# Performance work log

Measured on AMD Instinct MI355X. Metric: run time of the kernel, lower is better.

The kernel has to match this reference:

```python
import jax, jax.numpy as jnp
import numpy as np

N_NODES = 100000
N_EDGES = 3200000
ALPHA_KCL = 1.0
ALPHA_KVL = 1.0
EPS = 1e-6


def setup_inputs() -> dict:
    key = jax.random.key(0)
    k1, k2, k3, k4 = jax.random.split(key, 4)
    node_features = jax.random.normal(k1, (N_NODES, 4), dtype=jnp.float32)
    edge_index = jax.random.randint(k2, (2, N_EDGES), 0, N_NODES, dtype=jnp.int64)
    edge_logits = jax.random.normal(k3, (N_EDGES,), dtype=jnp.float32)
    edge_params = jax.random.uniform(k4, (N_EDGES, 2), dtype=jnp.float32)
    return {
        "node_features": node_features,
        "edge_index": edge_index,
        "edge_logits": edge_logits,
        "edge_params": edge_params,
    }


def reference(node_features, edge_index, edge_logits, edge_params):
    n_nodes = node_features.shape[0]
    edge_probs = jax.nn.sigmoid(edge_logits)  # [E]
    src = edge_index[0]  # [E]
    dst = edge_index[1]  # [E]
    v = node_features[:, 0]  # [N] voltage column
    # per-edge current: |v_src - v_dst| / (R + X + eps) * prob
    v_diff = jnp.abs(v[src] - v[dst])
    impedance = edge_params[:, 0] + edge_params[:, 1]
    current = v_diff / (impedance + EPS) * edge_probs  # [E]
    # KCL: each edge subtracts its current at src, adds at dst
    node_sum = (
        jax.ops.segment_sum(current, dst, num_segments=n_nodes)
        - jax.ops.segment_sum(current, src, num_segments=n_nodes)
    )  # [N]
    kcl_loss = jnp.mean(node_sum ** 2)
    # KVL (simplified): mean of per-column unbiased variance of edge_params
    kvl_loss = jnp.var(edge_params, axis=0, ddof=1).mean()
    return ALPHA_KCL * kcl_loss + ALPHA_KVL * kvl_loss
```

## Files before the change

### kernel.cpp

```cpp
#include <hip/hip_runtime.h>
#include <math.h>

#define N_NODES 100000
#define N_EDGES 3200000
#define EPS_F 1e-6f

#define SLICE_N 12500
#define NSLICE  8
#define NCHUNK  32
#define C_PAIRS (N_EDGES / 2 / NCHUNK)
#define SBATCH  8

#define NVARB   6250
#define NKCLB   391

#define CNT_WORD  32
#define PK_OFF    64
#define PART_OFF  (PK_OFF + 2 * N_EDGES)
#define VARP_OFF  (PART_OFF + NCHUNK * N_NODES)
#define KCLP_OFF  (VARP_OFF + 4 * NVARB)
#define WS_FLOATS (KCLP_OFF + NKCLB + 64)

__device__ __forceinline__ float wave_reduce(float v) {
    #pragma unroll
    for (int off = 32; off > 0; off >>= 1) v += __shfl_down(v, off, 64);
    return v;
}

__device__ __forceinline__ void fadd_agent(float* p, float v) {
    unsafeAtomicAdd(p, v);
}

__device__ __forceinline__ unsigned short f2bf(float f) {
    unsigned u = __float_as_uint(f);
    unsigned r = ((u >> 16) & 1u) + 0x7FFFu;
    return (unsigned short)((u + r) >> 16);
}
__device__ __forceinline__ float bf2f(unsigned short h) {
    return __uint_as_float(((unsigned)h) << 16);
}

__global__ __launch_bounds__(256) void prep_kernel(
    const float*  __restrict__ nf,
    const void*   __restrict__ eidx,
    const float*  __restrict__ logits,
    const float2* __restrict__ params,
    float*        __restrict__ ws)
{
    __shared__ float red[4][4];
    const int* i32 = (const int*)eidx;

    int any = 0;
    #pragma unroll
    for (int k = 1; k < 32; k += 2) any |= i32[k];
    const bool is32 = (any != 0);

    const int t = blockIdx.x * blockDim.x + threadIdx.x;

    if (t == 0) ((unsigned*)ws)[CNT_WORD] = 0;

    int2 sp, dp;
    if (is32) {
        sp = ((const int2*)i32)[t];
        dp = ((const int2*)(i32 + N_EDGES))[t];
    } else {
        const int4 a = ((const int4*)i32)[t];
        const int4 b = ((const int4*)(i32 + 2 * N_EDGES))[t];
        sp = make_int2(a.x, a.z);
        dp = make_int2(b.x, b.z);
    }

    const float vs0 = nf[sp.x * 4];
    const float vd0 = nf[dp.x * 4];
    const float vs1 = nf[sp.y * 4];
    const float vd1 = nf[dp.y * 4];

    const float4 pp = ((const float4*)params)[t];
    const float2 lg = ((const float2*)logits)[t];
    const float w0 = (1.0f / (1.0f + __expf(-lg.x))) / (pp.x + pp.y + EPS_F);
    const float w1 = (1.0f / (1.0f + __expf(-lg.y))) / (pp.z + pp.w + EPS_F);
    const float c0 = fabsf(vs0 - vd0) * w0;
    const float c1 = fabsf(vs1 - vd1) * w1;

    int4 pk;
    pk.x = (int)((unsigned)sp.x | ((unsigned)dp.x << 17));
    pk.y = (int)((((unsigned)dp.x) >> 15) | ((unsigned)f2bf(c0) << 2));
    pk.z = (int)((unsigned)sp.y | ((unsigned)dp.y << 17));
    pk.w = (int)((((unsigned)dp.y) >> 15) | ((unsigned)f2bf(c1) << 2));
    ((int4*)(ws + PK_OFF))[t] = pk;

    float s0 = pp.x + pp.z;
    float s1 = pp.y + pp.w;
    float q0 = pp.x * pp.x + pp.z * pp.z;
    float q1 = pp.y * pp.y + pp.w * pp.w;

    s0 = wave_reduce(s0); s1 = wave_reduce(s1);
    q0 = wave_reduce(q0); q1 = wave_reduce(q1);

    const int wid = threadIdx.x >> 6;
    if ((threadIdx.x & 63) == 0) {
        red[wid][0] = s0; red[wid][1] = s1; red[wid][2] = q0; red[wid][3] = q1;
    }
    __syncthreads();
    if (threadIdx.x == 0) {
        float4 o;
        o.x = red[0][0] + red[1][0] + red[2][0] + red[3][0];
        o.y = red[0][1] + red[1][1] + red[2][1] + red[3][1];
        o.z = red[0][2] + red[1][2] + red[2][2] + red[3][2];
        o.w = red[0][3] + red[1][3] + red[2][3] + red[3][3];
        ((float4*)(ws + VARP_OFF))[blockIdx.x] = o;
    }
}

__global__ __launch_bounds__(1024) void scatter_kernel(float* __restrict__ ws)
{
    __shared__ float bins[SLICE_N];

    const int c  = blockIdx.x & (NCHUNK - 1);
    const int s  = blockIdx.x >> 5;
    const unsigned lo = (unsigned)(s * SLICE_N);

    for (int j = threadIdx.x; j < SLICE_N; j += 1024) bins[j] = 0.f;
    __syncthreads();

    const int4* pk = (const int4*)(ws + PK_OFF);

    const int p0 = c * C_PAIRS;
    const int p1 = p0 + C_PAIRS;

    for (int base = p0 + (int)threadIdx.x; base < p1; base += 1024 * SBATCH) {
        int4 q[SBATCH];
        #pragma unroll
        for (int k = 0; k < SBATCH; ++k) {
            int p = base + k * 1024;
            p = (p < p1) ? p : (p1 - 1);
            q[k] = pk[p];
        }
        #pragma unroll
        for (int k = 0; k < SBATCH; ++k) {
            const int p = base + k * 1024;
            if (p < p1) {
                const unsigned lo0 = (unsigned)q[k].x, hi0 = (unsigned)q[k].y;
                const unsigned lo1 = (unsigned)q[k].z, hi1 = (unsigned)q[k].w;
                const unsigned s0 = (lo0 & 0x1FFFFu) - lo;
                const unsigned d0 = ((lo0 >> 17) | ((hi0 & 3u) << 15)) - lo;
                const unsigned s1 = (lo1 & 0x1FFFFu) - lo;
                const unsigned d1 = ((lo1 >> 17) | ((hi1 & 3u) << 15)) - lo;
                const float c0 = bf2f((unsigned short)((hi0 >> 2) & 0xFFFFu));
                const float c1 = bf2f((unsigned short)((hi1 >> 2) & 0xFFFFu));
                if (d0 < SLICE_N) atomicAdd(&bins[d0],  c0);
                if (s0 < SLICE_N) atomicAdd(&bins[s0], -c0);
                if (d1 < SLICE_N) atomicAdd(&bins[d1],  c1);
                if (s1 < SLICE_N) atomicAdd(&bins[s1], -c1);
            }
        }
    }
    __syncthreads();

    float4* pt4 = (float4*)(ws + PART_OFF + (size_t)c * N_NODES + lo);
    for (int j = threadIdx.x; j < SLICE_N / 4; j += 1024)
        pt4[j] = ((const float4*)bins)[j];
}

__global__ __launch_bounds__(256) void kclfinal_kernel(float* __restrict__ ws,
                                                       float* __restrict__ out)
{
    __shared__ float red[4];
    __shared__ unsigned last;

    const int i = blockIdx.x * blockDim.x + threadIdx.x;
    float acc = 0.f;
    if (i < N_NODES) {
        const float* p = ws + PART_OFF + i;
        float s = 0.f;
        #pragma unroll 8
        for (int c = 0; c < NCHUNK; ++c) s += p[(size_t)c * N_NODES];
        acc = s * s;
    }
    acc = wave_reduce(acc);
    if ((threadIdx.x & 63) == 0) red[threadIdx.x >> 6] = acc;
    __syncthreads();
    if (threadIdx.x == 0) {
        ws[KCLP_OFF + blockIdx.x] = red[0] + red[1] + red[2] + red[3];
        __threadfence();
        const unsigned old = atomicAdd((unsigned*)ws + CNT_WORD, 1u);
        last = (old == NKCLB - 1) ? 1u : 0u;
    }
    __syncthreads();
    if (!last) return;

    __shared__ float red2[4][5];
    float s0 = 0.f, s1 = 0.f, q0 = 0.f, q1 = 0.f, k = 0.f;

    const float4* vp = (const float4*)(ws + VARP_OFF);
    for (int j = threadIdx.x; j < NVARB; j += 256) {
        const float4 v = vp[j];
        s0 += v.x; s1 += v.y; q0 += v.z; q1 += v.w;
    }
    for (int j = threadIdx.x; j < NKCLB; j += 256)
        k += unsafeAtomicAdd(ws + KCLP_OFF + j, 0.0f);

    s0 = wave_reduce(s0); s1 = wave_reduce(s1);
    q0 = wave_reduce(q0); q1 = wave_reduce(q1);
    k  = wave_reduce(k);

    const int wid = threadIdx.x >> 6;
    if ((threadIdx.x & 63) == 0) {
        red2[wid][0] = s0; red2[wid][1] = s1; red2[wid][2] = q0;
        red2[wid][3] = q1; red2[wid][4] = k;
    }
    __syncthreads();
    if (threadIdx.x == 0) {
        float a0 = 0.f, a1 = 0.f, a2 = 0.f, a3 = 0.f, a4 = 0.f;
        #pragma unroll
        for (int w = 0; w < 4; ++w) {
            a0 += red2[w][0]; a1 += red2[w][1]; a2 += red2[w][2];
            a3 += red2[w][3]; a4 += red2[w][4];
        }
        const float n    = (float)N_EDGES;
        const float var0 = (a2 - a0 * a0 / n) / (n - 1.0f);
        const float var1 = (a3 - a1 * a1 / n) / (n - 1.0f);
        out[0] = a4 / (float)N_NODES + 0.5f * (var0 + var1);
    }
}

#define FB_NODE_OFF 64
__global__ __launch_bounds__(256) void edge_kernel_fb(
    const float*  __restrict__ nf,
    const void*   __restrict__ eidx,
    const float*  __restrict__ logits,
    const float2* __restrict__ params,
    float*        __restrict__ ws)
{
    const int*       i32 = (const int*)eidx;
    const long long* i64 = (const long long*)eidx;
    int any = 0;
    #pragma unroll
    for (int k = 1; k < 32; k += 2) any |= i32[k];
    const bool is32 = (any != 0);

    float* node_sum = ws + FB_NODE_OFF;
    float* acc      = ws + 1;

    float s0 = 0.f, s1 = 0.f, q0 = 0.f, q1 = 0.f;
    const int tid    = blockIdx.x * blockDim.x + threadIdx.x;
    const int stride = gridDim.x * blockDim.x;
    for (int i = tid; i < N_EDGES; i += stride) {
        int src, dst;
        if (is32) { src = i32[i]; dst = i32[N_EDGES + i]; }
        else      { src = (int)i64[i]; dst = (int)i64[N_EDGES + i]; }
        const float2 ep = params[i];
        const float  p  = 1.0f / (1.0f + __expf(-logits[i]));
        const float cur = fabsf(nf[src * 4] - nf[dst * 4]) / (ep.x + ep.y + EPS_F) * p;
        fadd_agent(node_sum + dst,  cur);
        fadd_agent(node_sum + src, -cur);
        s0 += ep.x; s1 += ep.y; q0 += ep.x * ep.x; q1 += ep.y * ep.y;
    }
    s0 = wave_reduce(s0); s1 = wave_reduce(s1);
    q0 = wave_reduce(q0); q1 = wave_reduce(q1);
    if ((threadIdx.x & 63) == 0) {
        fadd_agent(acc + 0, s0); fadd_agent(acc + 1, s1);
        fadd_agent(acc + 2, q0); fadd_agent(acc + 3, q1);
    }
}

__global__ __launch_bounds__(256) void kcl_kernel_fb(float* __restrict__ ws)
{
    const float* node_sum = ws + FB_NODE_OFF;
    float acc = 0.f;
    const int tid    = blockIdx.x * blockDim.x + threadIdx.x;
    const int stride = gridDim.x * blockDim.x;
    for (int i = tid; i < N_NODES; i += stride) {
        const float v = node_sum[i];
        acc += v * v;
    }
    acc = wave_reduce(acc);
    if ((threadIdx.x & 63) == 0) fadd_agent(ws + 5, acc);
}

__global__ void final_kernel_fb(const float* __restrict__ ws, float* __restrict__ out)
{
    const float s0 = ws[1], s1 = ws[2], q0 = ws[3], q1 = ws[4], k = ws[5];
    const float n  = (float)N_EDGES;
    const float var0 = (q0 - s0 * s0 / n) / (n - 1.0f);
    const float var1 = (q1 - s1 * s1 / n) / (n - 1.0f);
    out[0] = k / (float)N_NODES + 0.5f * (var0 + var1);
}

extern "C" void kernel_launch(void* const* d_in, const int* in_sizes, int n_in,
                              void* d_out, int out_size, void* d_ws, size_t ws_size,
                              hipStream_t stream) {
    const float*  nf     = (const float*)d_in[0];
    const void*   eidx   = d_in[1];
    const float*  logits = (const float*)d_in[2];
    const float2* params = (const float2*)d_in[3];
    float* ws  = (float*)d_ws;
    float* out = (float*)d_out;

    const size_t need = (size_t)WS_FLOATS * sizeof(float);

    if (ws_size >= need) {
        prep_kernel<<<NVARB, 256, 0, stream>>>(nf, eidx, logits, params, ws);
        scatter_kernel<<<NCHUNK * NSLICE, 1024, 0, stream>>>(ws);
        kclfinal_kernel<<<NKCLB, 256, 0, stream>>>(ws, out);
    } else {
        hipMemsetAsync(d_ws, 0, 256 + (size_t)N_NODES * sizeof(float), stream);
        edge_kernel_fb<<<2048, 256, 0, stream>>>(nf, eidx, logits, params, ws);
        kcl_kernel_fb<<<200, 256, 0, stream>>>(ws);
        final_kernel_fb<<<1, 1, 0, stream>>>(ws, out);
    }
}
```

Measured before the change: 186.1 us.

## Bucket edge contributions by node slice in prep instead of packed edge list

The prep kernel now computes each edge's bf16 current and appends per-endpoint 32-bit entries (value, sign, local index) into per-(chunk, slice) global buckets, staged through shared-memory lists and flushed with one global atomic per slice. The scatter kernel then reads only its own bucket rather than rescanning the whole packed edge array eight times, once per slice. This cuts scatter read traffic and filtering work, at the cost of shared atomics, a memset for the counters, and a larger workspace with fixed capacities. Bucket overflow beyond the capacity silently drops entries, which is a correctness risk if the index distribution is skewed.

```diff
diff --git a/kernel.cpp b/kernel.cpp
--- a/kernel.cpp
+++ b/kernel.cpp
@@ -4,21 +4,29 @@
 #define N_NODES 100000
 #define N_EDGES 3200000
 #define EPS_F 1e-6f
-
+#define PAIRS   (N_EDGES / 2)
+
+#define PPT        2
+#define PREP_T     256
+#define PREP_PAIRS (PREP_T * PPT)
+#define NPREPB     (PAIRS / PREP_PAIRS)
+#define LCAP       512
+
+#define NCHUNK  25
+#define NSLICE  8
 #define SLICE_N 12500
-#define NSLICE  8
-#define NCHUNK  32
-#define C_PAIRS (N_EDGES / 2 / NCHUNK)
-#define SBATCH  8
-
-#define NVARB   6250
+#define PB_PER_CHUNK (NPREPB / NCHUNK)
+#define BCAP    49152
+#define NBUCK   (NCHUNK * NSLICE)
+
 #define NKCLB   391
 
-#define CNT_WORD  32
-#define PK_OFF    64
-#define PART_OFF  (PK_OFF + 2 * N_EDGES)
+#define CTR_OFF   0
+#define CNT_WORD  200
+#define BUCK_OFF  256
+#define PART_OFF  (BUCK_OFF + NBUCK * BCAP)
 #define VARP_OFF  (PART_OFF + NCHUNK * N_NODES)
-#define KCLP_OFF  (VARP_OFF + 4 * NVARB)
+#define KCLP_OFF  (VARP_OFF + 4 * NPREPB)
 #define WS_FLOATS (KCLP_OFF + NKCLB + 64)
 
 __device__ __forceinline__ float wave_reduce(float v) {
@@ -47,7 +55,11 @@
     const float2* __restrict__ params,
     float*        __restrict__ ws)
 {
-    __shared__ float red[4][4];
+    __shared__ unsigned lists[NSLICE][LCAP];
+    __shared__ unsigned lcnt[NSLICE];
+    __shared__ unsigned lbase[NSLICE];
+    __shared__ float    red[4][4];
+
     const int* i32 = (const int*)eidx;
 
     int any = 0;
@@ -55,44 +67,96 @@
     for (int k = 1; k < 32; k += 2) any |= i32[k];
     const bool is32 = (any != 0);
 
-    const int t = blockIdx.x * blockDim.x + threadIdx.x;
-
-    if (t == 0) ((unsigned*)ws)[CNT_WORD] = 0;
-
-    int2 sp, dp;
+    if (threadIdx.x < NSLICE) lcnt[threadIdx.x] = 0;
+    __syncthreads();
+
+    const int t0 = blockIdx.x * PREP_PAIRS + threadIdx.x;
+    const int t1 = t0 + PREP_T;
+    const int chunk = blockIdx.x / PB_PER_CHUNK;
+
+    unsigned* gctr = (unsigned*)ws + CTR_OFF;
+    unsigned* buck = (unsigned*)(ws + BUCK_OFF);
+
+    int2 sp0, dp0, sp1, dp1;
     if (is32) {
-        sp = ((const int2*)i32)[t];
-        dp = ((const int2*)(i32 + N_EDGES))[t];
+        sp0 = ((const int2*)i32)[t0];
+        sp1 = ((const int2*)i32)[t1];
+        dp0 = ((const int2*)(i32 + N_EDGES))[t0];
+        dp1 = ((const int2*)(i32 + N_EDGES))[t1];
     } else {
-        const int4 a = ((const int4*)i32)[t];
-        const int4 b = ((const int4*)(i32 + 2 * N_EDGES))[t];
-        sp = make_int2(a.x, a.z);
-        dp = make_int2(b.x, b.z);
-    }
-
-    const float vs0 = nf[sp.x * 4];
-    const float vd0 = nf[dp.x * 4];
-    const float vs1 = nf[sp.y * 4];
-    const float vd1 = nf[dp.y * 4];
-
-    const float4 pp = ((const float4*)params)[t];
-    const float2 lg = ((const float2*)logits)[t];
-    const float w0 = (1.0f / (1.0f + __expf(-lg.x))) / (pp.x + pp.y + EPS_F);
-    const float w1 = (1.0f / (1.0f + __expf(-lg.y))) / (pp.z + pp.w + EPS_F);
-    const float c0 = fabsf(vs0 - vd0) * w0;
-    const float c1 = fabsf(vs1 - vd1) * w1;
-
-    int4 pk;
-    pk.x = (int)((unsigned)sp.x | ((unsigned)dp.x << 17));
-    pk.y = (int)((((unsigned)dp.x) >> 15) | ((unsigned)f2bf(c0) << 2));
-    pk.z = (int)((unsigned)sp.y | ((unsigned)dp.y << 17));
-    pk.w = (int)((((unsigned)dp.y) >> 15) | ((unsigned)f2bf(c1) << 2));
-    ((int4*)(ws + PK_OFF))[t] = pk;
-
-    float s0 = pp.x + pp.z;
-    float s1 = pp.y + pp.w;
-    float q0 = pp.x * pp.x + pp.z * pp.z;
-    float q1 = pp.y * pp.y + pp.w * pp.w;
+        const int4 a0 = ((const int4*)i32)[t0];
+        const int4 a1 = ((const int4*)i32)[t1];
+        const int4 b0 = ((const int4*)(i32 + 2 * N_EDGES))[t0];
+        const int4 b1 = ((const int4*)(i32 + 2 * N_EDGES))[t1];
+        sp0 = make_int2(a0.x, a0.z);  sp1 = make_int2(a1.x, a1.z);
+        dp0 = make_int2(b0.x, b0.z);  dp1 = make_int2(b1.x, b1.z);
+    }
+
+    const float vs00 = nf[sp0.x * 4];
+    const float vd00 = nf[dp0.x * 4];
+    const float vs01 = nf[sp0.y * 4];
+    const float vd01 = nf[dp0.y * 4];
+    const float vs10 = nf[sp1.x * 4];
+    const float vd10 = nf[dp1.x * 4];
+    const float vs11 = nf[sp1.y * 4];
+    const float vd11 = nf[dp1.y * 4];
+
+    const float4 pp0 = ((const float4*)params)[t0];
+    const float4 pp1 = ((const float4*)params)[t1];
+    const float2 lg0 = ((const float2*)logits)[t0];
+    const float2 lg1 = ((const float2*)logits)[t1];
+
+    const float w00 = (1.0f / (1.0f + __expf(-lg0.x))) / (pp0.x + pp0.y + EPS_F);
+    const float w01 = (1.0f / (1.0f + __expf(-lg0.y))) / (pp0.z + pp0.w + EPS_F);
+    const float w10 = (1.0f / (1.0f + __expf(-lg1.x))) / (pp1.x + pp1.y + EPS_F);
+    const float w11 = (1.0f / (1.0f + __expf(-lg1.y))) / (pp1.z + pp1.w + EPS_F);
+
+    const unsigned cb00 = f2bf(fabsf(vs00 - vd00) * w00);
+    const unsigned cb01 = f2bf(fabsf(vs01 - vd01) * w01);
+    const unsigned cb10 = f2bf(fabsf(vs10 - vd10) * w10);
+    const unsigned cb11 = f2bf(fabsf(vs11 - vd11) * w11);
+
+    #define APPEND(id, curbf, neg) do {                                        \
+        const unsigned s_  = (unsigned)(id) / SLICE_N;                         \
+        const unsigned e_  = ((curbf) << 16) | ((neg) << 14)                   \
+                             | ((unsigned)(id) - s_ * SLICE_N);                \
+        const unsigned ix_ = atomicAdd(&lcnt[s_], 1u);                         \
+        if (ix_ < LCAP) lists[s_][ix_] = e_;                                   \
+        else {               \
+            const unsigned g_ = atomicAdd(&gctr[chunk * NSLICE + s_], 1u);     \
+            if (g_ < BCAP) buck[(chunk * NSLICE + s_) * BCAP + g_] = e_;       \
+        }                                                                      \
+    } while (0)
+
+    APPEND(dp0.x, cb00, 0u);  APPEND(sp0.x, cb00, 1u);
+    APPEND(dp0.y, cb01, 0u);  APPEND(sp0.y, cb01, 1u);
+    APPEND(dp1.x, cb10, 0u);  APPEND(sp1.x, cb10, 1u);
+    APPEND(dp1.y, cb11, 0u);  APPEND(sp1.y, cb11, 1u);
+    #undef APPEND
+
+    __syncthreads();
+    if (threadIdx.x < NSLICE) {
+        unsigned n = lcnt[threadIdx.x];
+        if (n > LCAP) n = LCAP;
+        lcnt[threadIdx.x]  = n;
+        lbase[threadIdx.x] = atomicAdd(&gctr[chunk * NSLICE + threadIdx.x], n);
+    }
+    __syncthreads();
+
+    #pragma unroll
+    for (int s = 0; s < NSLICE; ++s) {
+        const unsigned n = lcnt[s], b = lbase[s];
+        unsigned* seg = buck + (chunk * NSLICE + s) * BCAP;
+        for (unsigned j = threadIdx.x; j < n; j += PREP_T) {
+            const unsigned slot = b + j;
+            if (slot < BCAP) seg[slot] = lists[s][j];
+        }
+    }
+
+    float s0 = pp0.x + pp0.z + pp1.x + pp1.z;
+    float s1 = pp0.y + pp0.w + pp1.y + pp1.w;
+    float q0 = pp0.x * pp0.x + pp0.z * pp0.z + pp1.x * pp1.x + pp1.z * pp1.z;
+    float q1 = pp0.y * pp0.y + pp0.w * pp0.w + pp1.y * pp1.y + pp1.w * pp1.w;
 
     s0 = wave_reduce(s0); s1 = wave_reduce(s1);
     q0 = wave_reduce(q0); q1 = wave_reduce(q1);
@@ -116,48 +180,38 @@
 {
     __shared__ float bins[SLICE_N];
 
-    const int c  = blockIdx.x & (NCHUNK - 1);
-    const int s  = blockIdx.x >> 5;
-    const unsigned lo = (unsigned)(s * SLICE_N);
+    const int c = blockIdx.x >> 3;
+    const int s = blockIdx.x & 7;
+
+    const unsigned* gctr = (const unsigned*)ws + CTR_OFF;
+    unsigned cnt = gctr[c * NSLICE + s];
+    if (cnt > BCAP) cnt = BCAP;
+    const unsigned* seg = (const unsigned*)(ws + BUCK_OFF) + (size_t)(c * NSLICE + s) * BCAP;
 
     for (int j = threadIdx.x; j < SLICE_N; j += 1024) bins[j] = 0.f;
     __syncthreads();
 
-    const int4* pk = (const int4*)(ws + PK_OFF);
-
-    const int p0 = c * C_PAIRS;
-    const int p1 = p0 + C_PAIRS;
-
-    for (int base = p0 + (int)threadIdx.x; base < p1; base += 1024 * SBATCH) {
-        int4 q[SBATCH];
+    for (unsigned base = threadIdx.x; base < cnt; base += 1024u * 8u) {
+        unsigned q[8];
         #pragma unroll
-        for (int k = 0; k < SBATCH; ++k) {
-            int p = base + k * 1024;
-            p = (p < p1) ? p : (p1 - 1);
-            q[k] = pk[p];
+        for (int k = 0; k < 8; ++k) {
+            unsigned p = base + (unsigned)k * 1024u;
+            p = (p < cnt) ? p : (cnt - 1u);
+            q[k] = seg[p];
         }
         #pragma unroll
-        for (int k = 0; k < SBATCH; ++k) {
-            const int p = base + k * 1024;
-            if (p < p1) {
-                const unsigned lo0 = (unsigned)q[k].x, hi0 = (unsigned)q[k].y;
-                const unsigned lo1 = (unsigned)q[k].z, hi1 = (unsigned)q[k].w;
-                const unsigned s0 = (lo0 & 0x1FFFFu) - lo;
-                const unsigned d0 = ((lo0 >> 17) | ((hi0 & 3u) << 15)) - lo;
-                const unsigned s1 = (lo1 & 0x1FFFFu) - lo;
-                const unsigned d1 = ((lo1 >> 17) | ((hi1 & 3u) << 15)) - lo;
-                const float c0 = bf2f((unsigned short)((hi0 >> 2) & 0xFFFFu));
-                const float c1 = bf2f((unsigned short)((hi1 >> 2) & 0xFFFFu));
-                if (d0 < SLICE_N) atomicAdd(&bins[d0],  c0);
-                if (s0 < SLICE_N) atomicAdd(&bins[s0], -c0);
-                if (d1 < SLICE_N) atomicAdd(&bins[d1],  c1);
-                if (s1 < SLICE_N) atomicAdd(&bins[s1], -c1);
+        for (int k = 0; k < 8; ++k) {
+            const unsigned p = base + (unsigned)k * 1024u;
+            if (p < cnt) {
+                const unsigned e = q[k];
+                const float v = __uint_as_float((e & 0xFFFF0000u) ^ ((e << 17) & 0x80000000u));
+                atomicAdd(&bins[e & 0x3FFFu], v);
             }
         }
     }
     __syncthreads();
 
-    float4* pt4 = (float4*)(ws + PART_OFF + (size_t)c * N_NODES + lo);
+    float4* pt4 = (float4*)(ws + PART_OFF + (size_t)c * N_NODES + s * SLICE_N);
     for (int j = threadIdx.x; j < SLICE_N / 4; j += 1024)
         pt4[j] = ((const float4*)bins)[j];
 }
@@ -173,7 +227,7 @@
     if (i < N_NODES) {
         const float* p = ws + PART_OFF + i;
         float s = 0.f;
-        #pragma unroll 8
+        #pragma unroll 5
         for (int c = 0; c < NCHUNK; ++c) s += p[(size_t)c * N_NODES];
         acc = s * s;
     }
@@ -193,7 +247,7 @@
     float s0 = 0.f, s1 = 0.f, q0 = 0.f, q1 = 0.f, k = 0.f;
 
     const float4* vp = (const float4*)(ws + VARP_OFF);
-    for (int j = threadIdx.x; j < NVARB; j += 256) {
+    for (int j = threadIdx.x; j < NPREPB; j += 256) {
         const float4 v = vp[j];
         s0 += v.x; s1 += v.y; q0 += v.z; q1 += v.w;
     }
@@ -300,8 +354,9 @@
     const size_t need = (size_t)WS_FLOATS * sizeof(float);
 
     if (ws_size >= need) {
-        prep_kernel<<<NVARB, 256, 0, stream>>>(nf, eidx, logits, params, ws);
-        scatter_kernel<<<NCHUNK * NSLICE, 1024, 0, stream>>>(ws);
+        hipMemsetAsync(d_ws, 0, 1024, stream);
+        prep_kernel<<<NPREPB, 256, 0, stream>>>(nf, eidx, logits, params, ws);
+        scatter_kernel<<<NBUCK, 1024, 0, stream>>>(ws);
         kclfinal_kernel<<<NKCLB, 256, 0, stream>>>(ws, out);
     } else {
         hipMemsetAsync(d_ws, 0, 256 + (size_t)N_NODES * sizeof(float), stream);
```

Measured after the change: 196.2 us. 5.5% more time.

## Pack voltages to bf16 and cache them in LDS for the edge gather

Applied to the files above, without the earlier changes.

A new pack kernel first compresses the voltage column into a bf16 array. The prep kernel then becomes a persistent grid-stride kernel with 256 blocks of 1024 threads. Each block copies the first 80000 voltages into LDS, serves gathers for those nodes from shared memory, and falls back to global memory for the rest. Each thread processes two pairs per iteration to expose more memory-level parallelism, and variance partials are written per wave instead of per block. This adds a kernel launch and rounds voltages to bf16 before differencing, which changes the precision of the per-edge currents.

```diff
diff --git a/kernel.cpp b/kernel.cpp
--- a/kernel.cpp
+++ b/kernel.cpp
@@ -4,6 +4,12 @@
 #define N_NODES 100000
 #define N_EDGES 3200000
 #define EPS_F 1e-6f
+#define PAIRS   (N_EDGES / 2)
+
+#define TBL_N   80000
+#define GNB     256
+#define GSTRIDE (GNB * 1024)
+#define NVARW   (GNB * 16)
 
 #define SLICE_N 12500
 #define NSLICE  8
@@ -11,15 +17,16 @@
 #define C_PAIRS (N_EDGES / 2 / NCHUNK)
 #define SBATCH  8
 
-#define NVARB   6250
 #define NKCLB   391
+#define NPACKB  196
 
 #define CNT_WORD  32
 #define PK_OFF    64
 #define PART_OFF  (PK_OFF + 2 * N_EDGES)
 #define VARP_OFF  (PART_OFF + NCHUNK * N_NODES)
-#define KCLP_OFF  (VARP_OFF + 4 * NVARB)
-#define WS_FLOATS (KCLP_OFF + NKCLB + 64)
+#define KCLP_OFF  (VARP_OFF + 4 * NVARW)
+#define VBF_OFF   (KCLP_OFF + 512)
+#define WS_FLOATS (VBF_OFF + N_NODES / 2 + 64)
 
 __device__ __forceinline__ float wave_reduce(float v) {
     #pragma unroll
@@ -40,75 +47,113 @@
     return __uint_as_float(((unsigned)h) << 16);
 }
 
-__global__ __launch_bounds__(256) void prep_kernel(
-    const float*  __restrict__ nf,
+__global__ __launch_bounds__(256) void pack_kernel(
+    const float* __restrict__ nf, float* __restrict__ ws)
+{
+    const int t = blockIdx.x * 256 + threadIdx.x;
+    if (t == 0) ((unsigned*)ws)[CNT_WORD] = 0;
+    if (t < N_NODES / 2) {
+        const float4 a = ((const float4*)nf)[2 * t];
+        const float4 b = ((const float4*)nf)[2 * t + 1];
+        ((unsigned*)(ws + VBF_OFF))[t] = (unsigned)f2bf(a.x) | ((unsigned)f2bf(b.x) << 16);
+    }
+}
+
+__global__ __launch_bounds__(1024, 4) void prep_kernel(
     const void*   __restrict__ eidx,
     const float*  __restrict__ logits,
     const float2* __restrict__ params,
     float*        __restrict__ ws)
 {
-    __shared__ float red[4][4];
+    __shared__ unsigned vlds[TBL_N / 2];
+
+    const unsigned* vsrc = (const unsigned*)(ws + VBF_OFF);
+    for (int j = threadIdx.x; j < TBL_N / 2; j += 1024) vlds[j] = vsrc[j];
+
     const int* i32 = (const int*)eidx;
-
     int any = 0;
     #pragma unroll
     for (int k = 1; k < 32; k += 2) any |= i32[k];
     const bool is32 = (any != 0);
 
-    const int t = blockIdx.x * blockDim.x + threadIdx.x;
-
-    if (t == 0) ((unsigned*)ws)[CNT_WORD] = 0;
-
-    int2 sp, dp;
-    if (is32) {
-        sp = ((const int2*)i32)[t];
-        dp = ((const int2*)(i32 + N_EDGES))[t];
-    } else {
-        const int4 a = ((const int4*)i32)[t];
-        const int4 b = ((const int4*)(i32 + 2 * N_EDGES))[t];
-        sp = make_int2(a.x, a.z);
-        dp = make_int2(b.x, b.z);
-    }
-
-    const float vs0 = nf[sp.x * 4];
-    const float vd0 = nf[dp.x * 4];
-    const float vs1 = nf[sp.y * 4];
-    const float vd1 = nf[dp.y * 4];
-
-    const float4 pp = ((const float4*)params)[t];
-    const float2 lg = ((const float2*)logits)[t];
-    const float w0 = (1.0f / (1.0f + __expf(-lg.x))) / (pp.x + pp.y + EPS_F);
-    const float w1 = (1.0f / (1.0f + __expf(-lg.y))) / (pp.z + pp.w + EPS_F);
-    const float c0 = fabsf(vs0 - vd0) * w0;
-    const float c1 = fabsf(vs1 - vd1) * w1;
-
-    int4 pk;
-    pk.x = (int)((unsigned)sp.x | ((unsigned)dp.x << 17));
-    pk.y = (int)((((unsigned)dp.x) >> 15) | ((unsigned)f2bf(c0) << 2));
-    pk.z = (int)((unsigned)sp.y | ((unsigned)dp.y << 17));
-    pk.w = (int)((((unsigned)dp.y) >> 15) | ((unsigned)f2bf(c1) << 2));
-    ((int4*)(ws + PK_OFF))[t] = pk;
-
-    float s0 = pp.x + pp.z;
-    float s1 = pp.y + pp.w;
-    float q0 = pp.x * pp.x + pp.z * pp.z;
-    float q1 = pp.y * pp.y + pp.w * pp.w;
+    __syncthreads();
+    const unsigned short* vl = (const unsigned short*)vlds;
+    const unsigned short* vg = (const unsigned short*)(ws + VBF_OFF);
+
+    const int gtid = blockIdx.x * 1024 + threadIdx.x;
+    int4* pk = (int4*)(ws + PK_OFF);
+
+    float s0 = 0.f, s1 = 0.f, q0 = 0.f, q1 = 0.f;
+
+    #define VGET(id) bf2f(((unsigned)(id) < TBL_N) ? vl[id] : vg[id])
+
+    for (int p = gtid; p < PAIRS; p += 2 * GSTRIDE) {
+        const int pb  = p + GSTRIDE;
+        const int pbc = (pb < PAIRS) ? pb : p;
+
+        int2 spA, dpA, spB, dpB;
+        if (is32) {
+            spA = ((const int2*)i32)[p];
+            spB = ((const int2*)i32)[pbc];
+            dpA = ((const int2*)(i32 + N_EDGES))[p];
+            dpB = ((const int2*)(i32 + N_EDGES))[pbc];
+        } else {
+            const int4 a0 = ((const int4*)i32)[p];
+            const int4 a1 = ((const int4*)i32)[pbc];
+            const int4 b0 = ((const int4*)(i32 + 2 * N_EDGES))[p];
+            const int4 b1 = ((const int4*)(i32 + 2 * N_EDGES))[pbc];
+            spA = make_int2(a0.x, a0.z);  spB = make_int2(a1.x, a1.z);
+            dpA = make_int2(b0.x, b0.z);  dpB = make_int2(b1.x, b1.z);
+        }
+        const float4 ppA = ((const float4*)params)[p];
+        const float4 ppB = ((const float4*)params)[pbc];
+        const float2 lgA = ((const float2*)logits)[p];
+        const float2 lgB = ((const float2*)logits)[pbc];
+
+        const float vsA0 = VGET(spA.x), vdA0 = VGET(dpA.x);
+        const float vsA1 = VGET(spA.y), vdA1 = VGET(dpA.y);
+        const float vsB0 = VGET(spB.x), vdB0 = VGET(dpB.x);
+        const float vsB1 = VGET(spB.y), vdB1 = VGET(dpB.y);
+
+        const float wA0 = (1.0f / (1.0f + __expf(-lgA.x))) / (ppA.x + ppA.y + EPS_F);
+        const float wA1 = (1.0f / (1.0f + __expf(-lgA.y))) / (ppA.z + ppA.w + EPS_F);
+        const float wB0 = (1.0f / (1.0f + __expf(-lgB.x))) / (ppB.x + ppB.y + EPS_F);
+        const float wB1 = (1.0f / (1.0f + __expf(-lgB.y))) / (ppB.z + ppB.w + EPS_F);
+
+        const float cA0 = fabsf(vsA0 - vdA0) * wA0;
+        const float cA1 = fabsf(vsA1 - vdA1) * wA1;
+        const float cB0 = fabsf(vsB0 - vdB0) * wB0;
+        const float cB1 = fabsf(vsB1 - vdB1) * wB1;
+
+        int4 oA, oB;
+        oA.x = (int)((unsigned)spA.x | ((unsigned)dpA.x << 17));
+        oA.y = (int)((((unsigned)dpA.x) >> 15) | ((unsigned)f2bf(cA0) << 2));
+        oA.z = (int)((unsigned)spA.y | ((unsigned)dpA.y << 17));
+        oA.w = (int)((((unsigned)dpA.y) >> 15) | ((unsigned)f2bf(cA1) << 2));
+        oB.x = (int)((unsigned)spB.x | ((unsigned)dpB.x << 17));
+        oB.y = (int)((((unsigned)dpB.x) >> 15) | ((unsigned)f2bf(cB0) << 2));
+        oB.z = (int)((unsigned)spB.y | ((unsigned)dpB.y << 17));
+        oB.w = (int)((((unsigned)dpB.y) >> 15) | ((unsigned)f2bf(cB1) << 2));
+
+        pk[p] = oA;
+        s0 += ppA.x + ppA.z;  s1 += ppA.y + ppA.w;
+        q0 += ppA.x * ppA.x + ppA.z * ppA.z;
+        q1 += ppA.y * ppA.y + ppA.w * ppA.w;
+        if (pb < PAIRS) {
+            pk[pb] = oB;
+            s0 += ppB.x + ppB.z;  s1 += ppB.y + ppB.w;
+            q0 += ppB.x * ppB.x + ppB.z * ppB.z;
+            q1 += ppB.y * ppB.y + ppB.w * ppB.w;
+        }
+    }
+    #undef VGET
 
     s0 = wave_reduce(s0); s1 = wave_reduce(s1);
     q0 = wave_reduce(q0); q1 = wave_reduce(q1);
 
-    const int wid = threadIdx.x >> 6;
     if ((threadIdx.x & 63) == 0) {
-        red[wid][0] = s0; red[wid][1] = s1; red[wid][2] = q0; red[wid][3] = q1;
-    }
-    __syncthreads();
-    if (threadIdx.x == 0) {
-        float4 o;
-        o.x = red[0][0] + red[1][0] + red[2][0] + red[3][0];
-        o.y = red[0][1] + red[1][1] + red[2][1] + red[3][1];
-        o.z = red[0][2] + red[1][2] + red[2][2] + red[3][2];
-        o.w = red[0][3] + red[1][3] + red[2][3] + red[3][3];
-        ((float4*)(ws + VARP_OFF))[blockIdx.x] = o;
+        float4 o; o.x = s0; o.y = s1; o.z = q0; o.w = q1;
+        ((float4*)(ws + VARP_OFF))[blockIdx.x * 16 + (threadIdx.x >> 6)] = o;
     }
 }
 
@@ -193,7 +238,7 @@
     float s0 = 0.f, s1 = 0.f, q0 = 0.f, q1 = 0.f, k = 0.f;
 
     const float4* vp = (const float4*)(ws + VARP_OFF);
-    for (int j = threadIdx.x; j < NVARB; j += 256) {
+    for (int j = threadIdx.x; j < NVARW; j += 256) {
         const float4 v = vp[j];
         s0 += v.x; s1 += v.y; q0 += v.z; q1 += v.w;
     }
@@ -300,7 +345,8 @@
     const size_t need = (size_t)WS_FLOATS * sizeof(float);
 
     if (ws_size >= need) {
-        prep_kernel<<<NVARB, 256, 0, stream>>>(nf, eidx, logits, params, ws);
+        pack_kernel<<<NPACKB, 256, 0, stream>>>(nf, ws);
+        prep_kernel<<<GNB, 1024, 0, stream>>>(eidx, logits, params, ws);
         scatter_kernel<<<NCHUNK * NSLICE, 1024, 0, stream>>>(ws);
         kclfinal_kernel<<<NKCLB, 256, 0, stream>>>(ws, out);
     } else {
```

New measurement: 169.6 us. 1.1x faster.
